# Optimization experiments

Hardware: AMD Instinct MI355X
Metric: run time of the kernel (lower is better)

The kernel has to match this reference:

```python
import jax, jax.numpy as jnp
import numpy as np

NT, NS, NH, NG = 365, 1024, 64, 32
NW = NH * 8 + 2


def setup_inputs() -> dict:
    key = jax.random.key(0)
    k1, k2, k3, k4 = jax.random.split(key, 4)
    std = 1.0 / np.sqrt(NH)
    x = jax.random.normal(k1, (NT, NS, 4), dtype=jnp.float32)
    # make P (precip) nonnegative and T1 < T2 plausible-ish; math is still generic
    xc = jax.random.normal(k2, (NS, NG), dtype=jnp.float32)
    fc_w = jax.random.uniform(k3, (NW, NG), minval=-std, maxval=std, dtype=jnp.float32)
    fc_b = jax.random.uniform(k4, (NW,), minval=-std, maxval=std, dtype=jnp.float32)
    return {"x": x, "xc": xc, "fc_w": fc_w, "fc_b": fc_b}


def reference(x, xc, fc_w, fc_b):
    nh = NH
    P, E, T1, T2 = x[..., 0], x[..., 1], x[..., 2], x[..., 3]  # each [nt, ns]
    Ta = (T1 + T2) * 0.5
    # rain/snow partition: rP = 1 - arccos((T1+T2)/(T2-T1))/3.1415, masked
    valid = (T1 < 0) & (T2 > 0)
    denom = jnp.where(valid, T2 - T1, 1.0)
    ratio = jnp.clip(jnp.where(valid, (T1 + T2) / denom, 0.0), -0.999999, 0.999999)
    rP = 1.0 - jnp.arccos(ratio) / 3.1415
    rP = jnp.where(T1 >= 0, 1.0, rP)
    rP = jnp.where(T2 <= 0, 0.0, rP)
    Ps = (1.0 - rP) * P  # snow   [nt, ns]
    Pl = rP * P          # liquid [nt, ns]

    w = xc @ fc_w.T + fc_b  # [ns, nh*8+2]
    gm = jnp.exp(w[:, :nh]) + 1.0
    ge = jax.nn.sigmoid(w[:, nh:2 * nh]) * 2.0
    go = jax.nn.sigmoid(w[:, 2 * nh:3 * nh])
    gl = jnp.exp(w[:, 3 * nh:4 * nh] * 2.0)
    ga = jax.nn.softmax(w[:, 4 * nh:5 * nh], axis=1)  # Dropout in eval mode = identity
    gb = jax.nn.sigmoid(w[:, 5 * nh:6 * nh])
    qb = jax.nn.relu(w[:, -1]) / nh  # [ns]
    kb = jax.nn.sigmoid(w[:, 6 * nh:7 * nh]) / 10.0
    gi = jax.nn.sigmoid(w[:, 7 * nh:8 * nh])

    ns = P.shape[1]
    init = (jnp.zeros((ns, nh), jnp.float32),) * 3  # S0, H0, G0

    def step(carry, inp):
        S0, H0, G0 = carry
        Ps_k, Pl_k, Ta_k, E_k = inp  # each [ns]
        S = S0 + Ps_k[:, None]
        Sm = jnp.minimum(S0, jax.nn.relu(Ta_k[:, None] * gm))  # snowmelt
        H = jax.nn.relu(H0 + Sm + Pl_k[:, None] * gi - E_k[:, None] * ge)
        Q1 = jax.nn.relu(H - gl)
        Q2a = jnp.minimum(H, gl) * go
        Q2 = Q2a * (1.0 - gb)
        G = G0 + Q2a * gb
        Q3 = G * kb
        H0n = jnp.minimum(H - Q2a, gl)
        G0n = G - Q3
        S0n = S - Sm
        Y = jnp.sum((Q1 + Q2 + Q3 + qb[:, None]) * ga, axis=1)  # [ns]
        return (S0n, H0n, G0n), Y

    _, Yout = jax.lax.scan(step, init, (Ps, Pl, Ta, E))
    return Yout  # [nt, ns]
```

## Files before the change

kernel.cpp:

```cpp
#include <hip/hip_runtime.h>
#include <math.h>

#define NT_ 365
#define NS_ 1024
#define NH_ 64
#define NG_ 32
#define NW_ 514
#define CH_ 64
#define NCHUNK_ 6
#define YPAD_ 65
#define WPB_ 8

__device__ __forceinline__ float sigmoidf(float v) {
  return 1.0f / (1.0f + expf(-v));
}

__device__ __forceinline__ float4 compute_met(float4 xv) {
  const float P = xv.x, E = xv.y, T1 = xv.z, T2 = xv.w;
  const float Ta = (T1 + T2) * 0.5f;
  float rP;
  if (T2 <= 0.0f) {
    rP = 0.0f;
  } else if (T1 >= 0.0f) {
    rP = 1.0f;
  } else {
    float r = (T1 + T2) / (T2 - T1);
    r = fminf(fmaxf(r, -0.999999f), 0.999999f);
    rP = 1.0f - acosf(r) * (1.0f / 3.1415f);
  }
  float4 m;
  m.x = (1.0f - rP) * P;
  m.y = rP * P;
  m.z = fmaxf(Ta, 0.0f);
  m.w = E;
  return m;
}

__global__ __launch_bounds__(512) void waternet_scan(
    const float* __restrict__ x,
    const float* __restrict__ xc,
    const float* __restrict__ fc_w,
    const float* __restrict__ fc_b,
    float* __restrict__ out)
{
  __shared__ float  ytile[WPB_][CH_ * YPAD_];
  __shared__ float4 smet[WPB_][CH_];

  const int tid  = threadIdx.x;
  const int lane = tid & 63;
  const int wv   = tid >> 6;
  const int site = (blockIdx.x << 3) + wv;
  const int us   = __builtin_amdgcn_readfirstlane(site);
  const float4* xp = (const float4*)x;

  float4 xcur = xp[lane * NS_ + site];

  float acc[8];
#pragma unroll
  for (int k = 0; k < 8; ++k) acc[k] = fc_b[k * NH_ + lane];
  float accq = fc_b[NW_ - 1];

  const float4* xcq = (const float4*)(xc + us * NG_);
  const float4* wq4 = (const float4*)fc_w;
#pragma unroll
  for (int g4 = 0; g4 < NG_ / 4; ++g4) {
    const float4 xv = xcq[g4];
#pragma unroll
    for (int k = 0; k < 8; ++k) {
      const float4 w = wq4[(k * NH_ + lane) * (NG_ / 4) + g4];
      acc[k] = fmaf(xv.x, w.x, acc[k]);
      acc[k] = fmaf(xv.y, w.y, acc[k]);
      acc[k] = fmaf(xv.z, w.z, acc[k]);
      acc[k] = fmaf(xv.w, w.w, acc[k]);
    }
    {
      const float4 w = wq4[(NW_ - 1) * (NG_ / 4) + g4];
      accq = fmaf(xv.x, w.x, accq);
      accq = fmaf(xv.y, w.y, accq);
      accq = fmaf(xv.z, w.z, accq);
      accq = fmaf(xv.w, w.w, accq);
    }
  }

  const float gm = expf(acc[0]) + 1.0f;
  const float ge = sigmoidf(acc[1]) * 2.0f;
  const float go = sigmoidf(acc[2]);
  const float gl = expf(acc[3] * 2.0f);
  float mx = acc[4];
#pragma unroll
  for (int mm = 32; mm >= 1; mm >>= 1) mx = fmaxf(mx, __shfl_xor(mx, mm, 64));
  const float ex = expf(acc[4] - mx);
  float sm = ex;
#pragma unroll
  for (int mm = 32; mm >= 1; mm >>= 1) sm += __shfl_xor(sm, mm, 64);
  const float ga = ex / sm;
  const float gb = sigmoidf(acc[5]);
  const float kb = sigmoidf(acc[6]) * 0.1f;
  const float gi = sigmoidf(acc[7]);
  const float qb = fmaxf(accq, 0.0f) * (1.0f / NH_);
  const float kb1m = 1.0f - kb;
  const float nge  = -ge;
  const float gq1  = go * (1.0f - gb) - 1.0f;

  float S0 = 0.0f, H0 = 0.0f, G0 = 0.0f;

  smet[wv][lane] = compute_met(xcur);

  auto step = [&](const float4 mt, float* ywaddr) {
    const float melt = mt.z * gm;
    const float dmx  = fmaxf(S0 - melt, 0.0f);
    const float hs   = H0 + S0;
    S0 = dmx + mt.x;
    const float t3 = fmaf(mt.y, gi, hs - dmx);
    const float H  = fmaxf(fmaf(mt.w, nge, t3), 0.0f);
    const float M  = fminf(H, gl);
    const float Q2a = M * go;
    H0 = fminf(H - Q2a, gl);
    const float G = fmaf(Q2a, gb, G0);
    G0 = G * kb1m;
    *ywaddr = fmaf(G, kb, fmaf(M, gq1, H)) * ga;
  };

  float*       yw = &ytile[wv][lane];
  const float* yr = &ytile[wv][lane * YPAD_];

  for (int c = 0; c < NCHUNK_; ++c) {
    int tn = (c + 1) * CH_ + lane;
    tn = (tn < NT_) ? tn : (NT_ - 1);
    const float4 xnext = xp[tn * NS_ + site];

    const float4* mp = &smet[wv][0];
#pragma unroll
    for (int j = 0; j < CH_; ++j) step(mp[j], yw + j * YPAD_);

    float r0 = 0.0f, r1 = 0.0f, r2 = 0.0f, r3 = 0.0f;
#pragma unroll
    for (int h = 0; h < CH_; h += 4) {
      r0 += yr[h + 0];
      r1 += yr[h + 1];
      r2 += yr[h + 2];
      r3 += yr[h + 3];
    }
    const int t_out = c * CH_ + lane;
    if (t_out < NT_) out[t_out * NS_ + site] = ((r0 + r1) + (r2 + r3)) + qb;

    if (c + 1 < NCHUNK_) smet[wv][lane] = compute_met(xnext);
  }
}

extern "C" void kernel_launch(void* const* d_in, const int* in_sizes, int n_in,
                              void* d_out, int out_size, void* d_ws, size_t ws_size,
                              hipStream_t stream) {
  const float* x    = (const float*)d_in[0];
  const float* xc   = (const float*)d_in[1];
  const float* fc_w = (const float*)d_in[2];
  const float* fc_b = (const float*)d_in[3];
  float* out = (float*)d_out;

  hipLaunchKernelGGL(waternet_scan, dim3(NS_ / WPB_), dim3(WPB_ * 64), 0, stream,
                     x, xc, fc_w, fc_b, out);
}
```

Measured before the change: 98.21 us.

## Replace LDS staging with readlane broadcasts and DPP wave reductions

Drops the shared-memory tiles used to broadcast forcing data and to transpose per-step outputs. Each step now reads the four forcing values with readlane and sums across the 64 lanes with a DPP add chain, taking the total from lane 63. This removes LDS traffic and the 64x64 transpose reduction, but adds a serial cross-lane reduction of about six DPP ops plus readlanes to every timestep. Those ops sit on the recurrence critical path.

```diff
diff --git a/kernel.cpp b/kernel.cpp
--- a/kernel.cpp
+++ b/kernel.cpp
@@ -8,11 +8,29 @@
 #define NW_ 514
 #define CH_ 64
 #define NCHUNK_ 6
-#define YPAD_ 65
 #define WPB_ 8
 
 __device__ __forceinline__ float sigmoidf(float v) {
   return 1.0f / (1.0f + expf(-v));
+}
+
+__device__ __forceinline__ float blane(float v, int j) {
+  return __int_as_float(__builtin_amdgcn_readlane(__float_as_int(v), j));
+}
+
+template<int CTRL>
+__device__ __forceinline__ float dpp_add(float x) {
+  int t = __builtin_amdgcn_update_dpp(0, __float_as_int(x), CTRL, 0xf, 0xf, true);
+  return x + __int_as_float(t);
+}
+__device__ __forceinline__ float wave_sum64(float x) {
+  x = dpp_add<0x111>(x);
+  x = dpp_add<0x112>(x);
+  x = dpp_add<0x114>(x);
+  x = dpp_add<0x118>(x);
+  x = dpp_add<0x142>(x);
+  x = dpp_add<0x143>(x);
+  return x;
 }
 
 __device__ __forceinline__ float4 compute_met(float4 xv) {
@@ -36,16 +54,13 @@
   return m;
 }
 
-__global__ __launch_bounds__(512) void waternet_scan(
+__global__ __launch_bounds__(WPB_ * 64) void waternet_scan(
     const float* __restrict__ x,
     const float* __restrict__ xc,
     const float* __restrict__ fc_w,
     const float* __restrict__ fc_b,
     float* __restrict__ out)
 {
-  __shared__ float  ytile[WPB_][CH_ * YPAD_];
-  __shared__ float4 smet[WPB_][CH_];
-
   const int tid  = threadIdx.x;
   const int lane = tid & 63;
   const int wv   = tid >> 6;
@@ -103,48 +118,44 @@
   const float gq1  = go * (1.0f - gb) - 1.0f;
 
   float S0 = 0.0f, H0 = 0.0f, G0 = 0.0f;
-
-  smet[wv][lane] = compute_met(xcur);
-
-  auto step = [&](const float4 mt, float* ywaddr) {
-    const float melt = mt.z * gm;
-    const float dmx  = fmaxf(S0 - melt, 0.0f);
-    const float hs   = H0 + S0;
-    S0 = dmx + mt.x;
-    const float t3 = fmaf(mt.y, gi, hs - dmx);
-    const float H  = fmaxf(fmaf(mt.w, nge, t3), 0.0f);
-    const float M  = fminf(H, gl);
-    const float Q2a = M * go;
-    H0 = fminf(H - Q2a, gl);
-    const float G = fmaf(Q2a, gb, G0);
-    G0 = G * kb1m;
-    *ywaddr = fmaf(G, kb, fmaf(M, gq1, H)) * ga;
-  };
-
-  float*       yw = &ytile[wv][lane];
-  const float* yr = &ytile[wv][lane * YPAD_];
+  float4 m = compute_met(xcur);
 
   for (int c = 0; c < NCHUNK_; ++c) {
     int tn = (c + 1) * CH_ + lane;
     tn = (tn < NT_) ? tn : (NT_ - 1);
     const float4 xnext = xp[tn * NS_ + site];
 
-    const float4* mp = &smet[wv][0];
+    float ycol = 0.0f;
 #pragma unroll
-    for (int j = 0; j < CH_; ++j) step(mp[j], yw + j * YPAD_);
+    for (int j = 0; j < CH_; ++j) {
+      const float Ps = blane(m.x, j);
+      const float Pl = blane(m.y, j);
+      const float Tr = blane(m.z, j);
+      const float E  = blane(m.w, j);
 
-    float r0 = 0.0f, r1 = 0.0f, r2 = 0.0f, r3 = 0.0f;
-#pragma unroll
-    for (int h = 0; h < CH_; h += 4) {
-      r0 += yr[h + 0];
-      r1 += yr[h + 1];
-      r2 += yr[h + 2];
-      r3 += yr[h + 3];
+      const float melt = Tr * gm;
+      const float Sm   = fminf(S0, melt);
+      const float base = H0 + Sm;
+      S0 = (S0 - Sm) + Ps;
+      const float t3 = fmaf(Pl, gi, base);
+      const float H  = fmaxf(fmaf(E, nge, t3), 0.0f);
+      const float M  = fminf(H, gl);
+      const float Q2a = M * go;
+      H0 = fminf(H - Q2a, gl);
+      const float G = fmaf(Q2a, gb, G0);
+      G0 = G * kb1m;
+      const float y = fmaf(G, kb, fmaf(M, gq1, H)) * ga;
+
+      const float tot = wave_sum64(y);
+      const float ts  = __int_as_float(
+          __builtin_amdgcn_readlane(__float_as_int(tot), 63));
+      ycol = (lane == j) ? ts : ycol;
     }
+
     const int t_out = c * CH_ + lane;
-    if (t_out < NT_) out[t_out * NS_ + site] = ((r0 + r1) + (r2 + r3)) + qb;
+    if (t_out < NT_) out[t_out * NS_ + site] = ycol + qb;
 
-    if (c + 1 < NCHUNK_) smet[wv][lane] = compute_met(xnext);
+    if (c + 1 < NCHUNK_) m = compute_met(xnext);
   }
 }
 
```

Result: slower. 118.3 us (+20.4%).

## Process two sites per wavefront with packed FP32 math in scan

Applied to the files above, without the earlier changes.

Each wavefront now handles two sites, so every lane carries a 2-wide vector of state and does the recurrence with packed fma/min/max operations. The shared-memory layouts for meteorology and partial outputs are reshaped to interleave the two sites, and the output is stored as float2. The block shrinks to 2 waves covering 4 sites, so the grid stays at 256 blocks but there are half as many waves in total. The aim is to get two independent recurrences per instruction and better ILP on the serial chain, at the cost of fewer resident waves for latency hiding.

```diff
diff --git a/kernel.cpp b/kernel.cpp
--- a/kernel.cpp
+++ b/kernel.cpp
@@ -8,11 +8,22 @@
 #define NW_ 514
 #define CH_ 64
 #define NCHUNK_ 6
-#define YPAD_ 65
-#define WPB_ 8
+#define YSTR_ 130
+
+typedef float v2 __attribute__((ext_vector_type(2)));
 
 __device__ __forceinline__ float sigmoidf(float v) {
   return 1.0f / (1.0f + expf(-v));
+}
+
+__device__ __forceinline__ v2 pk_fma(v2 a, v2 b, v2 c) {
+  return __builtin_elementwise_fma(a, b, c);
+}
+__device__ __forceinline__ v2 pk_min(v2 a, v2 b) {
+  return __builtin_elementwise_min(a, b);
+}
+__device__ __forceinline__ v2 pk_max(v2 a, v2 b) {
+  return __builtin_elementwise_max(a, b);
 }
 
 __device__ __forceinline__ float4 compute_met(float4 xv) {
@@ -36,115 +47,145 @@
   return m;
 }
 
-__global__ __launch_bounds__(512) void waternet_scan(
+__global__ __launch_bounds__(128) void waternet_scan(
     const float* __restrict__ x,
     const float* __restrict__ xc,
     const float* __restrict__ fc_w,
     const float* __restrict__ fc_b,
     float* __restrict__ out)
 {
-  __shared__ float  ytile[WPB_][CH_ * YPAD_];
-  __shared__ float4 smet[WPB_][CH_];
+  __shared__ float4 smet[2][2][CH_];
+  __shared__ float  ytile[2][CH_ * YSTR_];
 
   const int tid  = threadIdx.x;
   const int lane = tid & 63;
   const int wv   = tid >> 6;
-  const int site = (blockIdx.x << 3) + wv;
-  const int us   = __builtin_amdgcn_readfirstlane(site);
+  const int sA   = (blockIdx.x << 2) + (wv << 1);
+  const int usA  = __builtin_amdgcn_readfirstlane(sA);
   const float4* xp = (const float4*)x;
 
-  float4 xcur = xp[lane * NS_ + site];
-
-  float acc[8];
-#pragma unroll
-  for (int k = 0; k < 8; ++k) acc[k] = fc_b[k * NH_ + lane];
-  float accq = fc_b[NW_ - 1];
-
-  const float4* xcq = (const float4*)(xc + us * NG_);
-  const float4* wq4 = (const float4*)fc_w;
+  float4 xcA = xp[lane * NS_ + sA];
+  float4 xcB = xp[lane * NS_ + sA + 1];
+
+  v2 acc[8];
+#pragma unroll
+  for (int k = 0; k < 8; ++k) acc[k] = (v2)(fc_b[k * NH_ + lane]);
+  v2 accq = (v2)(fc_b[NW_ - 1]);
+
+  const float4* xcqA = (const float4*)(xc + usA * NG_);
+  const float4* xcqB = (const float4*)(xc + (usA + 1) * NG_);
+  const float4* wq4  = (const float4*)fc_w;
 #pragma unroll
   for (int g4 = 0; g4 < NG_ / 4; ++g4) {
-    const float4 xv = xcq[g4];
+    const float4 xa = xcqA[g4];
+    const float4 xb = xcqB[g4];
+    const v2 x0 = {xa.x, xb.x}, x1 = {xa.y, xb.y};
+    const v2 x2 = {xa.z, xb.z}, x3 = {xa.w, xb.w};
 #pragma unroll
     for (int k = 0; k < 8; ++k) {
       const float4 w = wq4[(k * NH_ + lane) * (NG_ / 4) + g4];
-      acc[k] = fmaf(xv.x, w.x, acc[k]);
-      acc[k] = fmaf(xv.y, w.y, acc[k]);
-      acc[k] = fmaf(xv.z, w.z, acc[k]);
-      acc[k] = fmaf(xv.w, w.w, acc[k]);
+      acc[k] = pk_fma(x0, (v2)(w.x), acc[k]);
+      acc[k] = pk_fma(x1, (v2)(w.y), acc[k]);
+      acc[k] = pk_fma(x2, (v2)(w.z), acc[k]);
+      acc[k] = pk_fma(x3, (v2)(w.w), acc[k]);
     }
     {
       const float4 w = wq4[(NW_ - 1) * (NG_ / 4) + g4];
-      accq = fmaf(xv.x, w.x, accq);
-      accq = fmaf(xv.y, w.y, accq);
-      accq = fmaf(xv.z, w.z, accq);
-      accq = fmaf(xv.w, w.w, accq);
-    }
-  }
-
-  const float gm = expf(acc[0]) + 1.0f;
-  const float ge = sigmoidf(acc[1]) * 2.0f;
-  const float go = sigmoidf(acc[2]);
-  const float gl = expf(acc[3] * 2.0f);
-  float mx = acc[4];
-#pragma unroll
-  for (int mm = 32; mm >= 1; mm >>= 1) mx = fmaxf(mx, __shfl_xor(mx, mm, 64));
-  const float ex = expf(acc[4] - mx);
-  float sm = ex;
-#pragma unroll
-  for (int mm = 32; mm >= 1; mm >>= 1) sm += __shfl_xor(sm, mm, 64);
-  const float ga = ex / sm;
-  const float gb = sigmoidf(acc[5]);
-  const float kb = sigmoidf(acc[6]) * 0.1f;
-  const float gi = sigmoidf(acc[7]);
-  const float qb = fmaxf(accq, 0.0f) * (1.0f / NH_);
-  const float kb1m = 1.0f - kb;
-  const float nge  = -ge;
-  const float gq1  = go * (1.0f - gb) - 1.0f;
-
-  float S0 = 0.0f, H0 = 0.0f, G0 = 0.0f;
-
-  smet[wv][lane] = compute_met(xcur);
-
-  auto step = [&](const float4 mt, float* ywaddr) {
-    const float melt = mt.z * gm;
-    const float dmx  = fmaxf(S0 - melt, 0.0f);
-    const float hs   = H0 + S0;
-    S0 = dmx + mt.x;
-    const float t3 = fmaf(mt.y, gi, hs - dmx);
-    const float H  = fmaxf(fmaf(mt.w, nge, t3), 0.0f);
-    const float M  = fminf(H, gl);
-    const float Q2a = M * go;
-    H0 = fminf(H - Q2a, gl);
-    const float G = fmaf(Q2a, gb, G0);
-    G0 = G * kb1m;
-    *ywaddr = fmaf(G, kb, fmaf(M, gq1, H)) * ga;
-  };
-
-  float*       yw = &ytile[wv][lane];
-  const float* yr = &ytile[wv][lane * YPAD_];
+      accq = pk_fma(x0, (v2)(w.x), accq);
+      accq = pk_fma(x1, (v2)(w.y), accq);
+      accq = pk_fma(x2, (v2)(w.z), accq);
+      accq = pk_fma(x3, (v2)(w.w), accq);
+    }
+  }
+
+  v2 gm, ge, go, gl, ga, gb, kb, gi;
+  {
+    gm = v2{expf(acc[0].x), expf(acc[0].y)} + (v2)(1.0f);
+    ge = v2{sigmoidf(acc[1].x), sigmoidf(acc[1].y)} * (v2)(2.0f);
+    go = v2{sigmoidf(acc[2].x), sigmoidf(acc[2].y)};
+    gl = v2{expf(acc[3].x * 2.0f), expf(acc[3].y * 2.0f)};
+    float mxa = acc[4].x, mxb = acc[4].y;
+#pragma unroll
+    for (int mm = 32; mm >= 1; mm >>= 1) {
+      mxa = fmaxf(mxa, __shfl_xor(mxa, mm, 64));
+      mxb = fmaxf(mxb, __shfl_xor(mxb, mm, 64));
+    }
+    const float exa = expf(acc[4].x - mxa), exb = expf(acc[4].y - mxb);
+    float sma = exa, smb = exb;
+#pragma unroll
+    for (int mm = 32; mm >= 1; mm >>= 1) {
+      sma += __shfl_xor(sma, mm, 64);
+      smb += __shfl_xor(smb, mm, 64);
+    }
+    ga = v2{exa / sma, exb / smb};
+    gb = v2{sigmoidf(acc[5].x), sigmoidf(acc[5].y)};
+    kb = v2{sigmoidf(acc[6].x), sigmoidf(acc[6].y)} * (v2)(0.1f);
+    gi = v2{sigmoidf(acc[7].x), sigmoidf(acc[7].y)};
+  }
+  const v2 qb   = pk_max(accq, (v2)(0.0f)) * (v2)(1.0f / NH_);
+  const v2 kb1m = (v2)(1.0f) - kb;
+  const v2 nge  = -ge;
+  const v2 gq1  = go * ((v2)(1.0f) - gb) - (v2)(1.0f);
+  const v2 zero = (v2)(0.0f);
+
+  v2 S0 = zero, H0 = zero, G0 = zero;
+
+  {
+    const float4 mA = compute_met(xcA);
+    const float4 mB = compute_met(xcB);
+    smet[wv][0][lane] = make_float4(mA.x, mB.x, mA.y, mB.y);
+    smet[wv][1][lane] = make_float4(mA.z, mB.z, mA.w, mB.w);
+  }
+
+  float* yrow = &ytile[wv][2 * lane];
+  const float* yred = &ytile[wv][lane * YSTR_];
 
   for (int c = 0; c < NCHUNK_; ++c) {
     int tn = (c + 1) * CH_ + lane;
     tn = (tn < NT_) ? tn : (NT_ - 1);
-    const float4 xnext = xp[tn * NS_ + site];
-
-    const float4* mp = &smet[wv][0];
-#pragma unroll
-    for (int j = 0; j < CH_; ++j) step(mp[j], yw + j * YPAD_);
-
-    float r0 = 0.0f, r1 = 0.0f, r2 = 0.0f, r3 = 0.0f;
-#pragma unroll
-    for (int h = 0; h < CH_; h += 4) {
-      r0 += yr[h + 0];
-      r1 += yr[h + 1];
-      r2 += yr[h + 2];
-      r3 += yr[h + 3];
-    }
+    const float4 xnA = xp[tn * NS_ + sA];
+    const float4 xnB = xp[tn * NS_ + sA + 1];
+
+    const float4* mp0 = &smet[wv][0][0];
+    const float4* mp1 = &smet[wv][1][0];
+#pragma unroll
+    for (int j = 0; j < CH_; ++j) {
+      const float4 a = mp0[j];
+      const float4 b = mp1[j];
+      const v2 Ps = {a.x, a.y}, Pl = {a.z, a.w};
+      const v2 Tr = {b.x, b.y}, E  = {b.z, b.w};
+
+      const v2 melt = Tr * gm;
+      const v2 Sm   = pk_min(S0, melt);
+      const v2 base = H0 + Sm;
+      S0 = (S0 - Sm) + Ps;
+      const v2 t3  = pk_fma(Pl, gi, base);
+      const v2 H   = pk_max(pk_fma(E, nge, t3), zero);
+      const v2 M   = pk_min(H, gl);
+      const v2 Q2a = M * go;
+      H0 = pk_min(H - Q2a, gl);
+      const v2 G = pk_fma(Q2a, gb, G0);
+      G0 = G * kb1m;
+      const v2 y = pk_fma(G, kb, pk_fma(M, gq1, H)) * ga;
+      *(v2*)&yrow[j * YSTR_] = y;
+    }
+
+    v2 r0 = zero, r1 = zero;
+#pragma unroll
+    for (int h = 0; h < CH_; h += 2) {
+      r0 += *(const v2*)&yred[2 * h];
+      r1 += *(const v2*)&yred[2 * h + 2];
+    }
+    const v2 tot = (r0 + r1) + qb;
     const int t_out = c * CH_ + lane;
-    if (t_out < NT_) out[t_out * NS_ + site] = ((r0 + r1) + (r2 + r3)) + qb;
-
-    if (c + 1 < NCHUNK_) smet[wv][lane] = compute_met(xnext);
+    if (t_out < NT_) *(v2*)(out + t_out * NS_ + sA) = tot;
+
+    if (c + 1 < NCHUNK_) {
+      const float4 mA = compute_met(xnA);
+      const float4 mB = compute_met(xnB);
+      smet[wv][0][lane] = make_float4(mA.x, mB.x, mA.y, mB.y);
+      smet[wv][1][lane] = make_float4(mA.z, mB.z, mA.w, mB.w);
+    }
   }
 }
 
@@ -157,6 +198,6 @@
   const float* fc_b = (const float*)d_in[3];
   float* out = (float*)d_out;
 
-  hipLaunchKernelGGL(waternet_scan, dim3(NS_ / WPB_), dim3(WPB_ * 64), 0, stream,
+  hipLaunchKernelGGL(waternet_scan, dim3(NS_ / 4), dim3(128), 0, stream,
                      x, xc, fc_w, fc_b, out);
 }
```

After: 95.94 us. -2.3%, faster.

## Halve block size, software-pipeline LDS met loads, restructure snowmelt step

Applied to the files above, without the earlier changes.

Blocks shrink from 8 to 4 wavefronts, so 256 blocks are launched instead of 128 and spread across more CUs. The per-chunk scan now prefetches the next 8 met records from LDS into registers while the current 8 steps run, which hides LDS latency behind the serial recurrence. The snowmelt update is also rewritten with an explicit min, closer to the reference form. The double buffers raise register use, and the outer chunk loop is no longer unrolled.

```diff
diff --git a/kernel.cpp b/kernel.cpp
--- a/kernel.cpp
+++ b/kernel.cpp
@@ -9,7 +9,7 @@
 #define CH_ 64
 #define NCHUNK_ 6
 #define YPAD_ 65
-#define WPB_ 8
+#define SUB_ 8
 
 __device__ __forceinline__ float sigmoidf(float v) {
   return 1.0f / (1.0f + expf(-v));
@@ -36,20 +36,20 @@
   return m;
 }
 
-__global__ __launch_bounds__(512) void waternet_scan(
+__global__ __launch_bounds__(256) void waternet_scan(
     const float* __restrict__ x,
     const float* __restrict__ xc,
     const float* __restrict__ fc_w,
     const float* __restrict__ fc_b,
     float* __restrict__ out)
 {
-  __shared__ float  ytile[WPB_][CH_ * YPAD_];
-  __shared__ float4 smet[WPB_][CH_];
+  __shared__ float4 smet[4][CH_];
+  __shared__ float  ytile[4][CH_ * YPAD_];
 
   const int tid  = threadIdx.x;
   const int lane = tid & 63;
   const int wv   = tid >> 6;
-  const int site = (blockIdx.x << 3) + wv;
+  const int site = (blockIdx.x << 2) + wv;
   const int us   = __builtin_amdgcn_readfirstlane(site);
   const float4* xp = (const float4*)x;
 
@@ -108,10 +108,10 @@
 
   auto step = [&](const float4 mt, float* ywaddr) {
     const float melt = mt.z * gm;
-    const float dmx  = fmaxf(S0 - melt, 0.0f);
-    const float hs   = H0 + S0;
-    S0 = dmx + mt.x;
-    const float t3 = fmaf(mt.y, gi, hs - dmx);
+    const float Sm   = fminf(S0, melt);
+    const float base = H0 + Sm;
+    S0 = (S0 - Sm) + mt.x;
+    const float t3 = fmaf(mt.y, gi, base);
     const float H  = fmaxf(fmaf(mt.w, nge, t3), 0.0f);
     const float M  = fminf(H, gl);
     const float Q2a = M * go;
@@ -124,14 +124,30 @@
   float*       yw = &ytile[wv][lane];
   const float* yr = &ytile[wv][lane * YPAD_];
 
+#pragma unroll 1
   for (int c = 0; c < NCHUNK_; ++c) {
     int tn = (c + 1) * CH_ + lane;
     tn = (tn < NT_) ? tn : (NT_ - 1);
     const float4 xnext = xp[tn * NS_ + site];
 
     const float4* mp = &smet[wv][0];
+
+    float4 mb0[SUB_], mb1[SUB_];
 #pragma unroll
-    for (int j = 0; j < CH_; ++j) step(mp[j], yw + j * YPAD_);
+    for (int u = 0; u < SUB_; ++u) mb0[u] = mp[u];
+
+#pragma unroll
+    for (int sc = 0; sc < CH_ / SUB_; ++sc) {
+      float4*       cur = (sc & 1) ? mb1 : mb0;
+      float4*       nxt = (sc & 1) ? mb0 : mb1;
+      if (sc < CH_ / SUB_ - 1) {
+#pragma unroll
+        for (int u = 0; u < SUB_; ++u) nxt[u] = mp[SUB_ * (sc + 1) + u];
+      }
+#pragma unroll
+      for (int u = 0; u < SUB_; ++u)
+        step(cur[u], yw + (SUB_ * sc + u) * YPAD_);
+    }
 
     float r0 = 0.0f, r1 = 0.0f, r2 = 0.0f, r3 = 0.0f;
 #pragma unroll
@@ -157,6 +173,6 @@
   const float* fc_b = (const float*)d_in[3];
   float* out = (float*)d_out;
 
-  hipLaunchKernelGGL(waternet_scan, dim3(NS_ / WPB_), dim3(WPB_ * 64), 0, stream,
+  hipLaunchKernelGGL(waternet_scan, dim3(NS_ / 4), dim3(256), 0, stream,
                      x, xc, fc_w, fc_b, out);
 }
```

New measurement: 88.32 us. -10.1%, faster.
